# Kernel tuning notes

Measured on AMD Instinct MI355X. Metric: run time of the kernel, lower is better.

Reference implementation:

```python
import jax, jax.numpy as jnp
import numpy as np
from jax import lax

# init_kwargs constants
DO_TUBE = False
TAU = 0.3
ITERATIONS = 5
BLEND_FACTOR = 0.3


def _avg_pool3(x):
    """3x3x3 avg pool, stride 1, zero padding 1, count_include_pad=True.
    x: (n, h, w, d). Matches torch F.avg_pool3d(kernel=3, stride=1, padding=1)."""
    s = lax.reduce_window(x, 0.0, lax.add, (1, 3, 3, 3), (1, 1, 1, 1), 'SAME')
    return s * (1.0 / 27.0)


def setup_inputs() -> dict:
    key = jax.random.key(0)
    # binary mask (b, 1, h, w, d) as docstring requires
    u = jax.random.uniform(key, (2, 1, 256, 256, 256), dtype=jnp.float32)
    seg = (u > 0.5).astype(jnp.float32)
    return {"segmentation": seg}


def reference(segmentation):
    b, c, h, w, d = segmentation.shape
    x = segmentation.reshape(b * c, h, w, d)

    # NOTE: in the original code `mask` is never updated inside the iteration
    # loop, so every iteration adds the identical term; the loop over the
    # batch dim is also trivially batchable. Compute the per-iteration term
    # once (fully batched) and scale by ITERATIONS.
    eroded = -_avg_pool3(-x)            # differentiable erosion
    dilated = _avg_pool3(eroded)        # differentiable dilation
    diff = x - dilated
    term = jax.nn.sigmoid((diff - 0.5) / TAU) + diff  # soft_threshold + residual
    skeleton = ITERATIONS * term

    skeleton = skeleton.reshape(b, c, h, w, d)
    # DO_TUBE is False (the torch code path for True is broken for 5D input)
    skeleton = BLEND_FACTOR * segmentation + (1.0 - BLEND_FACTOR) * skeleton
    skeleton = jnp.round(jnp.clip(skeleton, 0.0, 1.0))
    return 1.0 - skeleton
```

## Files before the change

kernel.cpp:

```cpp
#include <hip/hip_runtime.h>
#include <stdint.h>


typedef float vfloat4 __attribute__((ext_vector_type(4)));

#define CH 4
#define HB 4
#define NR 8
#define BLOCKS 2048

__device__ __forceinline__ uint32_t row_pack(uint32_t b, const int ln) {
    uint32_t up = (uint32_t)__builtin_amdgcn_update_dpp(
        0, (int)b, 0x138, 0xf, 0xf, true);
    uint32_t dn = (uint32_t)__builtin_amdgcn_update_dpp(
        0, (int)b, 0x130, 0xf, 0xf, true);
    uint64_t W = (uint64_t)(up >> 16) | ((uint64_t)b << 16)
               | ((uint64_t)(dn & 0xffffu) << 48);
    uint64_t S = W + ((W >> 8) << 1) + (W >> 16) * 3u + ((W >> 24) << 1) + (W >> 32);
    uint32_t n = (uint32_t)S;
    if (ln == 0)  n -= (b & 0xffu);
    if (ln == 63) n -= (b & 0xff000000u);
    return n | (b << 7);
}

__device__ __forceinline__ uint32_t bits_of(const vfloat4 v) {
    return (v.x > 0.5f ? 0x1u : 0u) | (v.y > 0.5f ? 0x100u : 0u)
         | (v.z > 0.5f ? 0x10000u : 0u) | (v.w > 0.5f ? 0x1000000u : 0u);
}

__global__ __launch_bounds__(256) void skel_fused(const float* __restrict__ x,
                                                  vfloat4* __restrict__ out) {
    const int ln  = threadIdx.x & 63;
    const int wid = (blockIdx.x << 2) | (threadIdx.x >> 6);
    const int wchunk =  wid        & 63;
    const int hblk   = (wid >> 6)  & 63;
    const int bi     =  wid >> 12;
    const int w0 = wchunk * CH;
    const int h0 = hblk * HB;

    const vfloat4* xb = (const vfloat4*)x + ((size_t)bi << 22);
    vfloat4* ob = out + ((size_t)bi << 22);

    uint32_t roff[NR];
    uint32_t rok[NR];
    #pragma unroll
    for (int r = 0; r < NR; ++r) {
        const int h  = h0 - 2 + r;
        const int hc = h < 0 ? 0 : (h > 255 ? 255 : h);
        roff[r] = (uint32_t)hc * 16384u;
        rok[r]  = (h >= 0 && h <= 255) ? 0xffffffffu : 0u;
    }

    auto ld = [&](int r, int wi) -> vfloat4 {
        const int wc = wi < 0 ? 0 : (wi > 255 ? 255 : wi);
        return xb[roff[r] + (uint32_t)wc * 64u + (uint32_t)ln];
    };
    auto pk = [&](vfloat4 v, int r, int wi) -> uint32_t {
        uint32_t b = bits_of(v);
        b = (wi >= 0 && wi < 256) ? b : 0u;
        return b & rok[r];
    };

    uint32_t win[NR][5];
    #pragma unroll
    for (int i = 0; i < 5; ++i) {
        vfloat4 tmp[NR];
        #pragma unroll
        for (int r = 0; r < NR; ++r) tmp[r] = ld(r, w0 - 2 + i);
        #pragma unroll
        for (int r = 0; r < NR; ++r)
            win[r][i] = row_pack(pk(tmp[r], r, w0 - 2 + i), ln);
    }
    vfloat4 nxt[NR];
    #pragma unroll
    for (int r = 0; r < NR; ++r) nxt[r] = ld(r, w0 + 3);

    #pragma unroll
    for (int j = 0; j < CH; ++j) {
        const int w = w0 + j;

        uint32_t t[NR];
        #pragma unroll
        for (int r = 0; r < NR; ++r) {
            const uint32_t m0 = win[r][0] & 0x7f7f7f7fu, m1 = win[r][1] & 0x7f7f7f7fu,
                           m2 = win[r][2] & 0x7f7f7f7fu, m3 = win[r][3] & 0x7f7f7f7fu,
                           m4 = win[r][4] & 0x7f7f7f7fu;
            uint32_t s = m0 + (m1 << 1) + m2 * 3u + (m3 << 1) + m4;
            if (w == 0 || w == 255) s -= m2;
            t[r] = s | (win[r][2] & 0x80808080u);
        }

        #pragma unroll
        for (int k = 0; k < HB; ++k) {
            const int h = h0 + k;
            const uint32_t m0 = t[k]   & 0x7f7f7f7fu, m1 = t[k+1] & 0x7f7f7f7fu,
                           m2 = t[k+2] & 0x7f7f7f7fu, m3 = t[k+3] & 0x7f7f7f7fu,
                           m4 = t[k+4] & 0x7f7f7f7fu;
            const uint32_t e0 = m0 & 0x00ff00ffu, e1 = m1 & 0x00ff00ffu,
                           e2 = m2 & 0x00ff00ffu, e3 = m3 & 0x00ff00ffu,
                           e4 = m4 & 0x00ff00ffu;
            const uint32_t o0 = (m0 >> 8) & 0x00ff00ffu, o1 = (m1 >> 8) & 0x00ff00ffu,
                           o2 = (m2 >> 8) & 0x00ff00ffu, o3 = (m3 >> 8) & 0x00ff00ffu,
                           o4 = (m4 >> 8) & 0x00ff00ffu;
            uint32_t ae = e0 + (e1 << 1) + e2 * 3u + (e3 << 1) + e4;
            uint32_t ao = o0 + (o1 << 1) + o2 * 3u + (o3 << 1) + o4;
            if (h == 0 || h == 255) { ae -= e2; ao -= o2; }
            const uint32_t xbit = t[k+2];
            vfloat4 o;
            o.x = ((ae & 0xffffu) >= 9u && !((xbit >> 7)  & 1u)) ? 1.0f : 0.0f;
            o.y = ((ao & 0xffffu) >= 9u && !((xbit >> 15) & 1u)) ? 1.0f : 0.0f;
            o.z = ((ae >> 16)     >= 9u && !((xbit >> 23) & 1u)) ? 1.0f : 0.0f;
            o.w = ((ao >> 16)     >= 9u && !((xbit >> 31) & 1u)) ? 1.0f : 0.0f;
            __builtin_nontemporal_store(
                o, &ob[(uint32_t)h * 16384u + (uint32_t)w * 64u + (uint32_t)ln]);
        }

        #pragma unroll
        for (int r = 0; r < NR; ++r) {
            const uint32_t rn = row_pack(pk(nxt[r], r, w + 3), ln);
            win[r][0] = win[r][1]; win[r][1] = win[r][2];
            win[r][2] = win[r][3]; win[r][3] = win[r][4];
            win[r][4] = rn;
        }
        if (j < CH - 1) {
            #pragma unroll
            for (int r = 0; r < NR; ++r) nxt[r] = ld(r, w + 4);
        }
    }
}

extern "C" void kernel_launch(void* const* d_in, const int* in_sizes, int n_in,
                              void* d_out, int out_size, void* d_ws, size_t ws_size,
                              hipStream_t stream) {
    const float* x = (const float*)d_in[0];
    (void)d_ws; (void)ws_size; (void)in_sizes; (void)n_in; (void)out_size;
    skel_fused<<<BLOCKS, 256, 0, stream>>>(x, (vfloat4*)d_out);
}
```

Measured before the change: 241.5 us.

## Share packed W-pass rows across waves through LDS with larger block tiles

Each block now computes a 16x8 (h,w) output tile. Four waves first pack and W-reduce 20 halo rows into shared memory, then each wave does the H-pass for 4 rows after a barrier. This cuts the redundant input loads and row packing that the old per-wave 4x4 tiles repeated across overlapping halos. In exchange it adds a block barrier, LDS traffic, higher register pressure from 12 in-flight loads, and halves the grid size.

```diff
diff --git a/kernel.cpp b/kernel.cpp
--- a/kernel.cpp
+++ b/kernel.cpp
@@ -4,10 +4,11 @@
 
 typedef float vfloat4 __attribute__((ext_vector_type(4)));
 
-#define CH 4
-#define HB 4
-#define NR 8
-#define BLOCKS 2048
+#define HB 16
+#define WB 8
+#define NR 20
+#define NC 12
+#define BLOCKS 1024
 
 __device__ __forceinline__ uint32_t row_pack(uint32_t b, const int ln) {
     uint32_t up = (uint32_t)__builtin_amdgcn_update_dpp(
@@ -28,74 +29,73 @@
          | (v.z > 0.5f ? 0x10000u : 0u) | (v.w > 0.5f ? 0x1000000u : 0u);
 }
 
-__global__ __launch_bounds__(256) void skel_fused(const float* __restrict__ x,
-                                                  vfloat4* __restrict__ out) {
-    const int ln  = threadIdx.x & 63;
-    const int wid = (blockIdx.x << 2) | (threadIdx.x >> 6);
-    const int wchunk =  wid        & 63;
-    const int hblk   = (wid >> 6)  & 63;
-    const int bi     =  wid >> 12;
-    const int w0 = wchunk * CH;
+__global__ __launch_bounds__(256) void skel_one(const float* __restrict__ x,
+                                                vfloat4* __restrict__ out) {
+    __shared__ uint32_t sm[NR * WB * 64];
+    const int ln = threadIdx.x & 63;
+    const int wv = threadIdx.x >> 6;
+    const int bid = blockIdx.x;
+    const int wchunk =  bid       & 31;
+    const int hblk   = (bid >> 5) & 15;
+    const int bi     =  bid >> 9;
+    const int w0 = wchunk * WB;
     const int h0 = hblk * HB;
 
     const vfloat4* xb = (const vfloat4*)x + ((size_t)bi << 22);
     vfloat4* ob = out + ((size_t)bi << 22);
 
-    uint32_t roff[NR];
-    uint32_t rok[NR];
+    const int r0 = wv * 5;
+    vfloat4 A[NC];
     #pragma unroll
-    for (int r = 0; r < NR; ++r) {
-        const int h  = h0 - 2 + r;
+    for (int rr = 0; rr < 5; ++rr) {
+        const int r = r0 + rr;
+        const int h = h0 - 2 + r;
         const int hc = h < 0 ? 0 : (h > 255 ? 255 : h);
-        roff[r] = (uint32_t)hc * 16384u;
-        rok[r]  = (h >= 0 && h <= 255) ? 0xffffffffu : 0u;
+        const uint32_t hok = (h >= 0 && h <= 255) ? 0xffffffffu : 0u;
+        #pragma unroll
+        for (int i = 0; i < NC; ++i) {
+            const int w = w0 - 2 + i;
+            const int wc = w < 0 ? 0 : (w > 255 ? 255 : w);
+            A[i] = xb[(uint32_t)hc * 16384u + (uint32_t)wc * 64u + (uint32_t)ln];
+        }
+        uint32_t p[NC];
+        #pragma unroll
+        for (int i = 0; i < NC; ++i) {
+            const int w = w0 - 2 + i;
+            uint32_t b = bits_of(A[i]);
+            b = (w >= 0 && w <= 255) ? (b & hok) : 0u;
+            p[i] = row_pack(b, ln);
+        }
+        #pragma unroll
+        for (int c = 0; c < WB; ++c) {
+            const int w = w0 + c;
+            const uint32_t m0 = p[c]   & 0x7f7f7f7fu, m1 = p[c+1] & 0x7f7f7f7fu,
+                           m2 = p[c+2] & 0x7f7f7f7fu, m3 = p[c+3] & 0x7f7f7f7fu,
+                           m4 = p[c+4] & 0x7f7f7f7fu;
+            uint32_t s = m0 + (m1 << 1) + m2 * 3u + (m3 << 1) + m4;
+            if (w == 0 || w == 255) s -= m2;
+            s |= (p[c+2] & 0x80808080u);
+            sm[((uint32_t)r * WB + (uint32_t)c) * 64u + (uint32_t)ln] = s;
+        }
     }
 
-    auto ld = [&](int r, int wi) -> vfloat4 {
-        const int wc = wi < 0 ? 0 : (wi > 255 ? 255 : wi);
-        return xb[roff[r] + (uint32_t)wc * 64u + (uint32_t)ln];
-    };
-    auto pk = [&](vfloat4 v, int r, int wi) -> uint32_t {
-        uint32_t b = bits_of(v);
-        b = (wi >= 0 && wi < 256) ? b : 0u;
-        return b & rok[r];
-    };
-
-    uint32_t win[NR][5];
-    #pragma unroll
-    for (int i = 0; i < 5; ++i) {
-        vfloat4 tmp[NR];
-        #pragma unroll
-        for (int r = 0; r < NR; ++r) tmp[r] = ld(r, w0 - 2 + i);
-        #pragma unroll
-        for (int r = 0; r < NR; ++r)
-            win[r][i] = row_pack(pk(tmp[r], r, w0 - 2 + i), ln);
-    }
-    vfloat4 nxt[NR];
-    #pragma unroll
-    for (int r = 0; r < NR; ++r) nxt[r] = ld(r, w0 + 3);
+    __syncthreads();
 
     #pragma unroll
-    for (int j = 0; j < CH; ++j) {
-        const int w = w0 + j;
-
-        uint32_t t[NR];
+    for (int kk = 0; kk < 4; ++kk) {
+        const int k = wv * 4 + kk;
+        const int h = h0 + k;
+        const bool hbnd = (h == 0 || h == 255);
         #pragma unroll
-        for (int r = 0; r < NR; ++r) {
-            const uint32_t m0 = win[r][0] & 0x7f7f7f7fu, m1 = win[r][1] & 0x7f7f7f7fu,
-                           m2 = win[r][2] & 0x7f7f7f7fu, m3 = win[r][3] & 0x7f7f7f7fu,
-                           m4 = win[r][4] & 0x7f7f7f7fu;
-            uint32_t s = m0 + (m1 << 1) + m2 * 3u + (m3 << 1) + m4;
-            if (w == 0 || w == 255) s -= m2;
-            t[r] = s | (win[r][2] & 0x80808080u);
-        }
-
-        #pragma unroll
-        for (int k = 0; k < HB; ++k) {
-            const int h = h0 + k;
-            const uint32_t m0 = t[k]   & 0x7f7f7f7fu, m1 = t[k+1] & 0x7f7f7f7fu,
-                           m2 = t[k+2] & 0x7f7f7f7fu, m3 = t[k+3] & 0x7f7f7f7fu,
-                           m4 = t[k+4] & 0x7f7f7f7fu;
+        for (int c = 0; c < WB; ++c) {
+            uint32_t q[5];
+            #pragma unroll
+            for (int s5 = 0; s5 < 5; ++s5)
+                q[s5] = sm[((uint32_t)(k + s5) * WB + (uint32_t)c) * 64u
+                           + (uint32_t)ln];
+            const uint32_t m0 = q[0] & 0x7f7f7f7fu, m1 = q[1] & 0x7f7f7f7fu,
+                           m2 = q[2] & 0x7f7f7f7fu, m3 = q[3] & 0x7f7f7f7fu,
+                           m4 = q[4] & 0x7f7f7f7fu;
             const uint32_t e0 = m0 & 0x00ff00ffu, e1 = m1 & 0x00ff00ffu,
                            e2 = m2 & 0x00ff00ffu, e3 = m3 & 0x00ff00ffu,
                            e4 = m4 & 0x00ff00ffu;
@@ -104,27 +104,16 @@
                            o4 = (m4 >> 8) & 0x00ff00ffu;
             uint32_t ae = e0 + (e1 << 1) + e2 * 3u + (e3 << 1) + e4;
             uint32_t ao = o0 + (o1 << 1) + o2 * 3u + (o3 << 1) + o4;
-            if (h == 0 || h == 255) { ae -= e2; ao -= o2; }
-            const uint32_t xbit = t[k+2];
+            if (hbnd) { ae -= e2; ao -= o2; }
+            const uint32_t cen = q[2];
             vfloat4 o;
-            o.x = ((ae & 0xffffu) >= 9u && !((xbit >> 7)  & 1u)) ? 1.0f : 0.0f;
-            o.y = ((ao & 0xffffu) >= 9u && !((xbit >> 15) & 1u)) ? 1.0f : 0.0f;
-            o.z = ((ae >> 16)     >= 9u && !((xbit >> 23) & 1u)) ? 1.0f : 0.0f;
-            o.w = ((ao >> 16)     >= 9u && !((xbit >> 31) & 1u)) ? 1.0f : 0.0f;
+            o.x = ((ae & 0xffffu) >= 9u && !((cen >> 7)  & 1u)) ? 1.0f : 0.0f;
+            o.y = ((ao & 0xffffu) >= 9u && !((cen >> 15) & 1u)) ? 1.0f : 0.0f;
+            o.z = ((ae >> 16)     >= 9u && !((cen >> 23) & 1u)) ? 1.0f : 0.0f;
+            o.w = ((ao >> 16)     >= 9u && !((cen >> 31) & 1u)) ? 1.0f : 0.0f;
             __builtin_nontemporal_store(
-                o, &ob[(uint32_t)h * 16384u + (uint32_t)w * 64u + (uint32_t)ln]);
-        }
-
-        #pragma unroll
-        for (int r = 0; r < NR; ++r) {
-            const uint32_t rn = row_pack(pk(nxt[r], r, w + 3), ln);
-            win[r][0] = win[r][1]; win[r][1] = win[r][2];
-            win[r][2] = win[r][3]; win[r][3] = win[r][4];
-            win[r][4] = rn;
-        }
-        if (j < CH - 1) {
-            #pragma unroll
-            for (int r = 0; r < NR; ++r) nxt[r] = ld(r, w + 4);
+                o, &ob[(uint32_t)h * 16384u + (uint32_t)(w0 + c) * 64u
+                       + (uint32_t)ln]);
         }
     }
 }
@@ -134,5 +123,5 @@
                               hipStream_t stream) {
     const float* x = (const float*)d_in[0];
     (void)d_ws; (void)ws_size; (void)in_sizes; (void)n_in; (void)out_size;
-    skel_fused<<<BLOCKS, 256, 0, stream>>>(x, (vfloat4*)d_out);
+    skel_one<<<BLOCKS, 256, 0, stream>>>(x, (vfloat4*)d_out);
 }
```

Result: no change. 240.0 us (-0.6%).

## Split into bit-pack prepass and packed-mask stencil kernel

Applied to the files above, without the earlier changes.

Adds a prepass kernel that reads the float mask once and writes one packed 32-bit word per four voxels, holding each voxel's d-direction neighbour sum and its centre bit, into the workspace. The main kernel then runs the w and h stencil passes on these compact words, computing one h row per wave over a 16-wide w strip, with a swizzled block order. The aim is to remove the repeated reads of full float halos from the fused kernel, since the halo traffic now touches a buffer about a quarter the size. In exchange it costs an extra launch, a workspace round trip of the packed buffer, and a five-row halo re-read in the main kernel.

```diff
diff --git a/kernel.cpp b/kernel.cpp
--- a/kernel.cpp
+++ b/kernel.cpp
@@ -4,10 +4,9 @@
 
 typedef float vfloat4 __attribute__((ext_vector_type(4)));
 
-#define CH 4
-#define HB 4
-#define NR 8
-#define BLOCKS 2048
+#define PRE_BLOCKS 2048
+#define CW 16
+#define MAIN_BLOCKS 2048
 
 __device__ __forceinline__ uint32_t row_pack(uint32_t b, const int ln) {
     uint32_t up = (uint32_t)__builtin_amdgcn_update_dpp(
@@ -28,103 +27,99 @@
          | (v.z > 0.5f ? 0x10000u : 0u) | (v.w > 0.5f ? 0x1000000u : 0u);
 }
 
-__global__ __launch_bounds__(256) void skel_fused(const float* __restrict__ x,
-                                                  vfloat4* __restrict__ out) {
+__global__ __launch_bounds__(256) void skel_pre(const float* __restrict__ x,
+                                                uint32_t* __restrict__ nd) {
     const int ln  = threadIdx.x & 63;
     const int wid = (blockIdx.x << 2) | (threadIdx.x >> 6);
-    const int wchunk =  wid        & 63;
-    const int hblk   = (wid >> 6)  & 63;
-    const int bi     =  wid >> 12;
-    const int w0 = wchunk * CH;
-    const int h0 = hblk * HB;
+    const vfloat4* xv = (const vfloat4*)x;
+    const uint32_t c0 = (uint32_t)wid * 16u;
+    #pragma unroll
+    for (int g = 0; g < 16; g += 4) {
+        vfloat4 v[4];
+        #pragma unroll
+        for (int i = 0; i < 4; ++i)
+            v[i] = xv[(c0 + (uint32_t)(g + i)) * 64u + (uint32_t)ln];
+        #pragma unroll
+        for (int i = 0; i < 4; ++i)
+            nd[(c0 + (uint32_t)(g + i)) * 64u + (uint32_t)ln] =
+                row_pack(bits_of(v[i]), ln);
+    }
+}
 
-    const vfloat4* xb = (const vfloat4*)x + ((size_t)bi << 22);
-    vfloat4* ob = out + ((size_t)bi << 22);
+__global__ __launch_bounds__(256) void skel_main(const uint32_t* __restrict__ nd,
+                                                 vfloat4* __restrict__ out) {
+    const int ln  = threadIdx.x & 63;
+    const int bid = (int)((blockIdx.x & 7u) * (MAIN_BLOCKS / 8) + (blockIdx.x >> 3));
+    const int wid = (bid << 2) | (threadIdx.x >> 6);
+    const int chunk = wid & 15;
+    const int slab  = wid >> 4;
+    const int hi    = slab & 255, bi = slab >> 8;
+    const int w0    = chunk * CW;
 
-    uint32_t roff[NR];
-    uint32_t rok[NR];
+    uint32_t rowbase[5];
+    uint32_t rmask[5];
     #pragma unroll
-    for (int r = 0; r < NR; ++r) {
-        const int h  = h0 - 2 + r;
-        const int hc = h < 0 ? 0 : (h > 255 ? 255 : h);
-        roff[r] = (uint32_t)hc * 16384u;
-        rok[r]  = (h >= 0 && h <= 255) ? 0xffffffffu : 0u;
+    for (int k = 0; k < 5; ++k) {
+        const int hk = hi - 2 + k;
+        const int hc = hk < 0 ? 0 : (hk > 255 ? 255 : hk);
+        rowbase[k] = ((uint32_t)bi * 256u + (uint32_t)hc) * 16384u + (uint32_t)ln;
+        rmask[k]   = (hk >= 0 && hk <= 255) ? 0xffffffffu : 0u;
     }
+    const bool hbnd = (hi == 0 || hi == 255);
+    const uint32_t obase = (uint32_t)slab * 16384u + (uint32_t)ln;
 
-    auto ld = [&](int r, int wi) -> vfloat4 {
-        const int wc = wi < 0 ? 0 : (wi > 255 ? 255 : wi);
-        return xb[roff[r] + (uint32_t)wc * 64u + (uint32_t)ln];
-    };
-    auto pk = [&](vfloat4 v, int r, int wi) -> uint32_t {
-        uint32_t b = bits_of(v);
-        b = (wi >= 0 && wi < 256) ? b : 0u;
-        return b & rok[r];
+    auto ldnd = [&](int k, int w) -> uint32_t {
+        if (w < 0 || w > 255) return 0u;
+        return nd[rowbase[k] + (uint32_t)w * 64u];
     };
 
-    uint32_t win[NR][5];
+    uint32_t cur[5][5];
     #pragma unroll
-    for (int i = 0; i < 5; ++i) {
-        vfloat4 tmp[NR];
+    for (int k = 0; k < 5; ++k)
         #pragma unroll
-        for (int r = 0; r < NR; ++r) tmp[r] = ld(r, w0 - 2 + i);
-        #pragma unroll
-        for (int r = 0; r < NR; ++r)
-            win[r][i] = row_pack(pk(tmp[r], r, w0 - 2 + i), ln);
-    }
-    vfloat4 nxt[NR];
-    #pragma unroll
-    for (int r = 0; r < NR; ++r) nxt[r] = ld(r, w0 + 3);
+        for (int i = 0; i < 5; ++i) cur[k][i] = ldnd(k, w0 - 2 + i);
 
     #pragma unroll
-    for (int j = 0; j < CH; ++j) {
+    for (int j = 0; j < CW; ++j) {
         const int w = w0 + j;
+        uint32_t nxt[5];
+        #pragma unroll
+        for (int k = 0; k < 5; ++k) nxt[k] = ldnd(k, w + 3);
 
-        uint32_t t[NR];
+        const uint32_t xb = cur[2][2];
+        uint32_t t[5];
         #pragma unroll
-        for (int r = 0; r < NR; ++r) {
-            const uint32_t m0 = win[r][0] & 0x7f7f7f7fu, m1 = win[r][1] & 0x7f7f7f7fu,
-                           m2 = win[r][2] & 0x7f7f7f7fu, m3 = win[r][3] & 0x7f7f7f7fu,
-                           m4 = win[r][4] & 0x7f7f7f7fu;
+        for (int k = 0; k < 5; ++k) {
+            const uint32_t m0 = cur[k][0] & 0x7f7f7f7fu,
+                           m1 = cur[k][1] & 0x7f7f7f7fu,
+                           m2 = cur[k][2] & 0x7f7f7f7fu,
+                           m3 = cur[k][3] & 0x7f7f7f7fu,
+                           m4 = cur[k][4] & 0x7f7f7f7fu;
             uint32_t s = m0 + (m1 << 1) + m2 * 3u + (m3 << 1) + m4;
             if (w == 0 || w == 255) s -= m2;
-            t[r] = s | (win[r][2] & 0x80808080u);
+            t[k] = s & rmask[k];
         }
+        const uint32_t e0 = t[0] & 0x00ff00ffu, e1 = t[1] & 0x00ff00ffu,
+                       e2 = t[2] & 0x00ff00ffu, e3 = t[3] & 0x00ff00ffu,
+                       e4 = t[4] & 0x00ff00ffu;
+        const uint32_t o0 = (t[0] >> 8) & 0x00ff00ffu, o1 = (t[1] >> 8) & 0x00ff00ffu,
+                       o2 = (t[2] >> 8) & 0x00ff00ffu, o3 = (t[3] >> 8) & 0x00ff00ffu,
+                       o4 = (t[4] >> 8) & 0x00ff00ffu;
+        uint32_t ae = e0 + (e1 << 1) + e2 * 3u + (e3 << 1) + e4;
+        uint32_t ao = o0 + (o1 << 1) + o2 * 3u + (o3 << 1) + o4;
+        if (hbnd) { ae -= e2; ao -= o2; }
+        vfloat4 o;
+        o.x = ((ae & 0xffffu) >= 9u && !((xb >> 7)  & 1u)) ? 1.0f : 0.0f;
+        o.y = ((ao & 0xffffu) >= 9u && !((xb >> 15) & 1u)) ? 1.0f : 0.0f;
+        o.z = ((ae >> 16)     >= 9u && !((xb >> 23) & 1u)) ? 1.0f : 0.0f;
+        o.w = ((ao >> 16)     >= 9u && !((xb >> 31) & 1u)) ? 1.0f : 0.0f;
+        __builtin_nontemporal_store(o, &out[obase + (uint32_t)w * 64u]);
 
         #pragma unroll
-        for (int k = 0; k < HB; ++k) {
-            const int h = h0 + k;
-            const uint32_t m0 = t[k]   & 0x7f7f7f7fu, m1 = t[k+1] & 0x7f7f7f7fu,
-                           m2 = t[k+2] & 0x7f7f7f7fu, m3 = t[k+3] & 0x7f7f7f7fu,
-                           m4 = t[k+4] & 0x7f7f7f7fu;
-            const uint32_t e0 = m0 & 0x00ff00ffu, e1 = m1 & 0x00ff00ffu,
-                           e2 = m2 & 0x00ff00ffu, e3 = m3 & 0x00ff00ffu,
-                           e4 = m4 & 0x00ff00ffu;
-            const uint32_t o0 = (m0 >> 8) & 0x00ff00ffu, o1 = (m1 >> 8) & 0x00ff00ffu,
-                           o2 = (m2 >> 8) & 0x00ff00ffu, o3 = (m3 >> 8) & 0x00ff00ffu,
-                           o4 = (m4 >> 8) & 0x00ff00ffu;
-            uint32_t ae = e0 + (e1 << 1) + e2 * 3u + (e3 << 1) + e4;
-            uint32_t ao = o0 + (o1 << 1) + o2 * 3u + (o3 << 1) + o4;
-            if (h == 0 || h == 255) { ae -= e2; ao -= o2; }
-            const uint32_t xbit = t[k+2];
-            vfloat4 o;
-            o.x = ((ae & 0xffffu) >= 9u && !((xbit >> 7)  & 1u)) ? 1.0f : 0.0f;
-            o.y = ((ao & 0xffffu) >= 9u && !((xbit >> 15) & 1u)) ? 1.0f : 0.0f;
-            o.z = ((ae >> 16)     >= 9u && !((xbit >> 23) & 1u)) ? 1.0f : 0.0f;
-            o.w = ((ao >> 16)     >= 9u && !((xbit >> 31) & 1u)) ? 1.0f : 0.0f;
-            __builtin_nontemporal_store(
-                o, &ob[(uint32_t)h * 16384u + (uint32_t)w * 64u + (uint32_t)ln]);
-        }
-
-        #pragma unroll
-        for (int r = 0; r < NR; ++r) {
-            const uint32_t rn = row_pack(pk(nxt[r], r, w + 3), ln);
-            win[r][0] = win[r][1]; win[r][1] = win[r][2];
-            win[r][2] = win[r][3]; win[r][3] = win[r][4];
-            win[r][4] = rn;
-        }
-        if (j < CH - 1) {
-            #pragma unroll
-            for (int r = 0; r < NR; ++r) nxt[r] = ld(r, w + 4);
+        for (int k = 0; k < 5; ++k) {
+            cur[k][0] = cur[k][1]; cur[k][1] = cur[k][2];
+            cur[k][2] = cur[k][3]; cur[k][3] = cur[k][4];
+            cur[k][4] = nxt[k];
         }
     }
 }
@@ -133,6 +128,7 @@
                               void* d_out, int out_size, void* d_ws, size_t ws_size,
                               hipStream_t stream) {
     const float* x = (const float*)d_in[0];
-    (void)d_ws; (void)ws_size; (void)in_sizes; (void)n_in; (void)out_size;
-    skel_fused<<<BLOCKS, 256, 0, stream>>>(x, (vfloat4*)d_out);
+    uint32_t* nd = (uint32_t*)d_ws;
+    skel_pre<<<PRE_BLOCKS, 256, 0, stream>>>(x, nd);
+    skel_main<<<MAIN_BLOCKS, 256, 0, stream>>>(nd, (vfloat4*)d_out);
 }
```

New measurement: 245.3 us. No clear change (+1.6%).
